# Kernel tuning notes

Measured on AMD Instinct MI355X. Metric: run time of the kernel, lower is better.

## Reference

```python
import jax, jax.numpy as jnp
import numpy as np
import math

K = 10  # args.k, hardcoded in order_topk/fast_topk

def sinusoid_pe(seq_len, d_model, dtype=jnp.float32):
    # PositionalEmbedding: pe[:,0::2]=sin(pos*div), pe[:,1::2]=cos(pos*div)
    pos = jnp.arange(seq_len, dtype=jnp.float32)[:, None]
    div = jnp.exp(jnp.arange(0, d_model, 2, dtype=jnp.float32) * (-math.log(10000.0) / d_model))
    ang = pos * div  # [S, d_model//2]
    pe = jnp.zeros((seq_len, d_model), dtype=jnp.float32)
    pe = pe.at[:, 0::2].set(jnp.sin(ang)).at[:, 1::2].set(jnp.cos(ang))
    return pe.astype(dtype)


def setup_inputs() -> dict:
    key = jax.random.key(0)
    ks = jax.random.split(key, 5)
    B, D, S = 128, 512, 512
    scale1 = 1.0 / math.sqrt(2 * D)
    scale2 = 1.0 / math.sqrt(D)
    return {
        "x": jax.random.normal(ks[0], (B, D, S), dtype=jnp.float32),
        "w1": jax.random.normal(ks[1], (2 * D, D), dtype=jnp.float32) * scale1,
        "b1": jax.random.normal(ks[2], (D,), dtype=jnp.float32) * scale1,
        "w2": jax.random.normal(ks[3], (D, 1), dtype=jnp.float32) * scale2,
        "b2": jax.random.normal(ks[4], (1,), dtype=jnp.float32) * scale2,
    }


def reference(x, w1, b1, w2, b2):
    # x: [B, D, S] -> feature: [B, S, D]  (Sampler: x = x.transpose(-1,-2))
    feat = jnp.swapaxes(x, -1, -2)
    B, S, D = feat.shape
    # shot == 1 branch: per-video mean over tokens, broadcast over seq
    info_g = jnp.broadcast_to(feat.mean(axis=-2, keepdims=True), feat.shape)
    h = jnp.concatenate([feat, info_g], axis=-1)  # [B, S, 2D]
    # evaluator: PositionalEmbedding(1024) -> Linear(1024,512) -> ReLU -> Linear(512,1)
    h = h + sinusoid_pe(S, 2 * D, h.dtype)[None]
    score = jax.nn.relu(jnp.einsum('bsf,fd->bsd', h, w1) + b1)
    score = (jnp.einsum('bsd,do->bso', score, w2) + b2)[..., 0]  # [B, S]
    mn = score.min(axis=1, keepdims=True)
    mx = score.max(axis=1, keepdims=True)
    norm_score = (score - mn) / (mx - mn + 1e-4)
    # fast_topk (eval path): top-k indices, sorted ascending, one-hot selection
    _, idx = jax.lax.top_k(norm_score, K)      # [B, K]
    idx = jnp.sort(idx, axis=-1)
    # torch: one_hot -> [B,K,S], .transpose(-1,-2) -> [B,S,K], then indices.transpose(-1,-2) -> [B,K,S]
    indices = jax.nn.one_hot(idx, S, dtype=feat.dtype)  # [B, K, S]
    selected_feature = jnp.einsum('bks,bsd->bkd', indices, feat)  # bmm gather
    return indices, selected_feature, feat
```

## Files before the change

kernel.cpp:

```cpp
#include <hip/hip_runtime.h>
#include <math.h>

#define B 128
#define D 512
#define S 512
#define TOPK 10

typedef short bf16x8 __attribute__((ext_vector_type(8)));
typedef unsigned short u16x8 __attribute__((ext_vector_type(8)));
typedef float f32x4 __attribute__((ext_vector_type(4)));


__device__ __forceinline__ unsigned splitf(float f) {
    unsigned u = __float_as_uint(f);
    unsigned rb = u + 0x7FFFu + ((u >> 16) & 1u);
    float hf = __uint_as_float(rb & 0xFFFF0000u);
    unsigned u2 = __float_as_uint(f - hf);
    return (rb >> 16) | (u2 & 0xFFFF0000u);
}

__device__ __forceinline__ size_t w1t_base(int d, int k) {
    return (size_t)(((d >> 8) * 32 + (k >> 5)) * 4 + ((k >> 3) & 3)) * 4096 +
           (size_t)(d & 255) * 16 + (k & 7);
}

__global__ __launch_bounds__(512) void fused_stage1(
    const float* __restrict__ x, float* __restrict__ feat, float* __restrict__ g_part,
    ushort* __restrict__ peh, ushort* __restrict__ pel,
    const float* __restrict__ w1, ushort* __restrict__ w1tsw) {
    __shared__ float tile[64 * 129];
    int bid = (int)blockIdx.x;
    int t = threadIdx.x;

    if (bid < 4096) {
        int b = bid >> 5;
        int d0 = ((bid >> 3) & 3) * 128;
        int sblk = bid & 7;
        int s0 = sblk * 64;
        int ty = t >> 4, tx = t & 15;
        const float4* x4 = (const float4*)(x + (size_t)b * D * S);
        float psum[4];
#pragma unroll
        for (int q = 0; q < 4; ++q) {
            int d = ty + 32 * q;
            float4 v = x4[(size_t)(d0 + d) * (S / 4) + (s0 >> 2) + tx];
            tile[d + (4 * tx + 0) * 129] = v.x;
            tile[d + (4 * tx + 1) * 129] = v.y;
            tile[d + (4 * tx + 2) * 129] = v.z;
            tile[d + (4 * tx + 3) * 129] = v.w;
            float sm = (v.x + v.y) + (v.z + v.w);
#pragma unroll
            for (int off = 8; off; off >>= 1) sm += __shfl_down(sm, off, 16);
            psum[q] = sm;
        }
        if (tx == 0) {
            float* gp = g_part + (size_t)sblk * 65536 + b * D + d0;
#pragma unroll
            for (int q = 0; q < 4; ++q) gp[ty + 32 * q] = psum[q] * (1.0f / S);
        }
        __syncthreads();
        int fx = t & 31, sy = t >> 5;
        float* fbase = feat + (size_t)b * S * D + d0 + 4 * fx;
#pragma unroll
        for (int j = 0; j < 4; ++j) {
            int s = sy + 16 * j;
            f32x4 o;
            o[0] = tile[(4 * fx + 0) + s * 129];
            o[1] = tile[(4 * fx + 1) + s * 129];
            o[2] = tile[(4 * fx + 2) + s * 129];
            o[3] = tile[(4 * fx + 3) + s * 129];
            __builtin_nontemporal_store(o, (f32x4*)(fbase + (size_t)(s0 + s) * D));
        }
    } else if (bid < 4608) {
        int s = bid - 4096;
        int i = t;
        float ei = expf((float)(2 * i) * -0.0089944730195f);
        float ang = (float)s * ei;
        float sv = sinf(ang), cv = cosf(ang);
        unsigned ps = splitf(sv), pc = splitf(cv);
        size_t base = (size_t)s * 1024 + 2 * i;
        peh[base] = (ushort)(ps & 0xFFFFu);
        peh[base + 1] = (ushort)(pc & 0xFFFFu);
        pel[base] = (ushort)(ps >> 16);
        pel[base + 1] = (ushort)(pc >> 16);
    } else {
        int id2 = bid - 4608;
        int rp = id2 & 1, tt = id2 >> 1;
        int m = t & 255;
        int c0 = (t >> 8) * 2;
        int d = rp * 256 + m;
        int hs = (m >> 2) & 1;
        ushort* outp = w1tsw + (size_t)(rp * 32 + tt) * 16384 + (size_t)m * 16;
#pragma unroll
        for (int cc = 0; cc < 2; ++cc) {
            int c = c0 + cc;
            u16x8 hi, lo;
#pragma unroll
            for (int j = 0; j < 8; ++j) {
                unsigned p = splitf(w1[(size_t)(tt * 32 + c * 8 + j) * D + d]);
                hi[j] = (ushort)(p & 0xFFFFu);
                lo[j] = (ushort)(p >> 16);
            }
            *(u16x8*)(outp + c * 4096 + hs * 8) = hi;
            *(u16x8*)(outp + c * 4096 + (hs ^ 1) * 8) = lo;
        }
    }
}

#define CP 40
__global__ __launch_bounds__(256) void fused_stage2(
    const float* __restrict__ g_part, const float* __restrict__ w1,
    float* __restrict__ gterm, float* __restrict__ score,
    const ushort* __restrict__ peh, const ushort* __restrict__ pel,
    const ushort* __restrict__ w1tsw, const float* __restrict__ b1,
    float* __restrict__ C1) {
    __shared__ short smemS[4 * 64 * CP];
    int bid = (int)blockIdx.x;
    int t = threadIdx.x;

    if (bid < 256) {
        score[bid * 256 + t] = 0.0f;
        int b = bid >> 1, half = bid & 1;
        float* gs = (float*)smemS;
#pragma unroll
        for (int h = 0; h < 2; ++h) {
            int k = h * 256 + t;
            float acc = 0.f;
#pragma unroll
            for (int sb = 0; sb < 8; ++sb) acc += g_part[(size_t)sb * 65536 + b * D + k];
            gs[k] = acc;
        }
        __syncthreads();
        int d = half * 256 + t;
        float a0 = 0.f, a1 = 0.f, a2 = 0.f, a3 = 0.f;
        for (int k = 0; k < 512; k += 4) {
            a0 += gs[k + 0] * w1[(size_t)(D + k + 0) * D + d];
            a1 += gs[k + 1] * w1[(size_t)(D + k + 1) * D + d];
            a2 += gs[k + 2] * w1[(size_t)(D + k + 2) * D + d];
            a3 += gs[k + 3] * w1[(size_t)(D + k + 3) * D + d];
        }
        gterm[b * D + d] = (a0 + a1) + (a2 + a3);
    } else {
        int cid = bid - 256;
        int d0 = (cid & 7) * 64, s0 = (cid >> 3) * 64;
        short* sAh = smemS;
        short* sAl = smemS + 64 * CP;
        short* sBh = smemS + 2 * 64 * CP;
        short* sBl = smemS + 3 * 64 * CP;
        int w = t >> 6, l = t & 63, lc = l & 15, lg = l >> 4;
        int tm = t >> 2, tk = (t & 3) * 8;
        int bhs = (tm >> 2) & 1;
        f32x4 acc[4] = {};
        for (int k0 = 0; k0 < 1024; k0 += 32) {
            __syncthreads();
            *(bf16x8*)(sAh + tm * CP + tk) =
                *(const bf16x8*)(peh + (size_t)(s0 + tm) * 1024 + k0 + tk);
            *(bf16x8*)(sAl + tm * CP + tk) =
                *(const bf16x8*)(pel + (size_t)(s0 + tm) * 1024 + k0 + tk);
            size_t boff = w1t_base(d0 + tm, k0 + tk);
            *(bf16x8*)(sBh + tm * CP + tk) = *(const bf16x8*)(w1tsw + boff + bhs * 8);
            *(bf16x8*)(sBl + tm * CP + tk) = *(const bf16x8*)(w1tsw + boff + (bhs ^ 1) * 8);
            __syncthreads();
            int m = w * 16 + lc;
            bf16x8 ah = *(const bf16x8*)(sAh + m * CP + lg * 8);
            bf16x8 al = *(const bf16x8*)(sAl + m * CP + lg * 8);
#pragma unroll
            for (int j = 0; j < 4; ++j) {
                int n = j * 16 + lc;
                bf16x8 bh = *(const bf16x8*)(sBh + n * CP + lg * 8);
                bf16x8 bl = *(const bf16x8*)(sBl + n * CP + lg * 8);
                acc[j] = __builtin_amdgcn_mfma_f32_16x16x32_bf16(ah, bh, acc[j], 0, 0, 0);
                acc[j] = __builtin_amdgcn_mfma_f32_16x16x32_bf16(ah, bl, acc[j], 0, 0, 0);
                acc[j] = __builtin_amdgcn_mfma_f32_16x16x32_bf16(al, bh, acc[j], 0, 0, 0);
            }
        }
#pragma unroll
        for (int j = 0; j < 4; ++j)
#pragma unroll
            for (int reg = 0; reg < 4; ++reg) {
                int sg = s0 + w * 16 + lg * 4 + reg;
                int dg = d0 + j * 16 + lc;
                C1[(size_t)sg * D + dg] = acc[j][reg] + b1[dg];
            }
    }
}

__device__ __forceinline__ void gload16(const void* src, void* dst) {
    __builtin_amdgcn_global_load_lds((const __attribute__((address_space(1))) void*)src,
                                     (__attribute__((address_space(3))) void*)dst, 16, 0, 0);
}

__device__ __forceinline__ void split_write(short* sAbuf, int am, int ahalf,
                                            float4 a0, float4 a1, float4 a2, float4 a3) {
    int hs = (am >> 2) & 1;
#pragma unroll
    for (int cc = 0; cc < 2; ++cc) {
        float e0, e1, e2, e3, e4, e5, e6, e7;
        if (cc == 0) {
            e0 = a0.x; e1 = a0.y; e2 = a0.z; e3 = a0.w;
            e4 = a1.x; e5 = a1.y; e6 = a1.z; e7 = a1.w;
        } else {
            e0 = a2.x; e1 = a2.y; e2 = a2.z; e3 = a2.w;
            e4 = a3.x; e5 = a3.y; e6 = a3.z; e7 = a3.w;
        }
        unsigned p0 = splitf(e0), p1 = splitf(e1), p2 = splitf(e2), p3 = splitf(e3);
        unsigned p4 = splitf(e4), p5 = splitf(e5), p6 = splitf(e6), p7 = splitf(e7);
        u16x8 hi, lo;
        hi[0] = (ushort)(p0 & 0xFFFFu); lo[0] = (ushort)(p0 >> 16);
        hi[1] = (ushort)(p1 & 0xFFFFu); lo[1] = (ushort)(p1 >> 16);
        hi[2] = (ushort)(p2 & 0xFFFFu); lo[2] = (ushort)(p2 >> 16);
        hi[3] = (ushort)(p3 & 0xFFFFu); lo[3] = (ushort)(p3 >> 16);
        hi[4] = (ushort)(p4 & 0xFFFFu); lo[4] = (ushort)(p4 >> 16);
        hi[5] = (ushort)(p5 & 0xFFFFu); lo[5] = (ushort)(p5 >> 16);
        hi[6] = (ushort)(p6 & 0xFFFFu); lo[6] = (ushort)(p6 >> 16);
        hi[7] = (ushort)(p7 & 0xFFFFu); lo[7] = (ushort)(p7 >> 16);
        short* dst = sAbuf + (size_t)(2 * ahalf + cc) * 4096 + (size_t)am * 16;
        *(u16x8*)(dst + hs * 8) = hi;
        *(u16x8*)(dst + (hs ^ 1) * 8) = lo;
    }
}

__global__ __launch_bounds__(512, 2) void gemm_mfma(
    const float* __restrict__ feat, const ushort* __restrict__ w1tsw,
    const float* __restrict__ w2, const float* __restrict__ gterm,
    const float* __restrict__ C1, float* __restrict__ score, int row_base) {
    __shared__ short sA[2][4][256][16];
    __shared__ short sB[2][4][256][16];
    int t = threadIdx.x;
    int id = (int)blockIdx.x;
    int lid = (id & 7) * 32 + (id >> 3);
    int rp = lid >> 1, cp = lid & 1;
    int row0 = row_base + (rp << 8);
    int d0 = cp << 8;
    int b = row0 >> 9;

    int am = t & 255, ahalf = t >> 8;
    const float4* asrc = (const float4*)(feat + (size_t)(row0 + am) * D + ahalf * 16);
    const ushort* btile = w1tsw + (size_t)(cp * 32) * 16384;
    int wv = t >> 6, l = t & 63, lc = l & 15, lg = l >> 4;
    int wr = wv >> 1, wc = wv & 1;
    int wbase = (t & ~63);
    int hs = (lc >> 2) & 1;
    int oh = hs * 8, ol = (hs ^ 1) * 8;

    f32x4 acc[4][8] = {};

    {
        float4 a0 = asrc[0], a1 = asrc[1], a2 = asrc[2], a3 = asrc[3];
#pragma unroll
        for (int q = 0; q < 4; ++q)
            gload16(btile + (size_t)(q * 512 + t) * 8,
                    &sB[0][0][0][0] + (size_t)(q * 512 + wbase) * 8);
        split_write(&sA[0][0][0][0], am, ahalf, a0, a1, a2, a3);
    }
    __syncthreads();

    for (int ts = 0; ts < 16; ++ts) {
        int cur = ts & 1, nxt = cur ^ 1;
        float4 a0, a1, a2, a3;
        if (ts < 15) {
            a0 = asrc[(ts + 1) * 8 + 0];
            a1 = asrc[(ts + 1) * 8 + 1];
            a2 = asrc[(ts + 1) * 8 + 2];
            a3 = asrc[(ts + 1) * 8 + 3];
#pragma unroll
            for (int q = 0; q < 4; ++q)
                gload16(btile + (size_t)(ts + 1) * 16384 + (size_t)(q * 512 + t) * 8,
                        &sB[nxt][0][0][0] + (size_t)(q * 512 + wbase) * 8);
        }
        bf16x8 ahf[4], alf[4];
#pragma unroll
        for (int i = 0; i < 4; ++i) {
            const short* ap = &sA[cur][lg][wr * 64 + i * 16 + lc][0];
            ahf[i] = *(const bf16x8*)(ap + oh);
            alf[i] = *(const bf16x8*)(ap + ol);
        }
        __builtin_amdgcn_s_setprio(1);
#pragma unroll
        for (int j = 0; j < 8; ++j) {
            const short* bp = &sB[cur][lg][wc * 128 + j * 16 + lc][0];
            bf16x8 bh = *(const bf16x8*)(bp + oh);
            bf16x8 bl = *(const bf16x8*)(bp + ol);
#pragma unroll
            for (int i = 0; i < 4; ++i) {
                acc[i][j] = __builtin_amdgcn_mfma_f32_16x16x32_bf16(ahf[i], bh, acc[i][j], 0, 0, 0);
                acc[i][j] = __builtin_amdgcn_mfma_f32_16x16x32_bf16(ahf[i], bl, acc[i][j], 0, 0, 0);
                acc[i][j] = __builtin_amdgcn_mfma_f32_16x16x32_bf16(alf[i], bh, acc[i][j], 0, 0, 0);
            }
        }
        __builtin_amdgcn_s_setprio(0);
        if (ts < 15) split_write(&sA[nxt][0][0][0], am, ahalf, a0, a1, a2, a3);
        __syncthreads();
    }

    float w2v[8], gt[8];
#pragma unroll
    for (int j = 0; j < 8; ++j) {
        int d = d0 + wc * 128 + j * 16 + lc;
        w2v[j] = w2[d];
        gt[j] = gterm[b * D + d];
    }
#pragma unroll
    for (int i = 0; i < 4; ++i)
#pragma unroll
        for (int reg = 0; reg < 4; ++reg) {
            int srow = row0 + wr * 64 + i * 16 + lg * 4 + reg;
            int s = srow & 511;
            float part = 0.f;
#pragma unroll
            for (int j = 0; j < 8; ++j) {
                int d = d0 + wc * 128 + j * 16 + lc;
                float z = acc[i][j][reg] + gt[j] + C1[(size_t)s * D + d];
                part += w2v[j] * fmaxf(z, 0.f);
            }
#pragma unroll
            for (int off = 8; off; off >>= 1) part += __shfl_down(part, off, 16);
            if (lc == 0) atomicAdd(&score[srow], part);
        }
}

__global__ void topk_kernel(const float* __restrict__ score, const float* __restrict__ feat,
                            float* __restrict__ out_ind, float* __restrict__ out_sel) {
    __shared__ float work[512];
    __shared__ float wvv[8];
    __shared__ int wii[8];
    __shared__ int topi[TOPK];
    int b = blockIdx.x, t = threadIdx.x;
    work[t] = score[b * S + t];
    __syncthreads();
    for (int it = 0; it < TOPK; ++it) {
        float v = work[t];
        int i = t;
#pragma unroll
        for (int off = 32; off; off >>= 1) {
            float ov = __shfl_down(v, off);
            int oi = __shfl_down(i, off);
            if (ov > v || (ov == v && oi < i)) { v = ov; i = oi; }
        }
        if ((t & 63) == 0) { wvv[t >> 6] = v; wii[t >> 6] = i; }
        __syncthreads();
        if (t == 0) {
            float bv = wvv[0];
            int bi = wii[0];
            for (int w = 1; w < 8; ++w)
                if (wvv[w] > bv || (wvv[w] == bv && wii[w] < bi)) { bv = wvv[w]; bi = wii[w]; }
            topi[it] = bi;
            work[bi] = -INFINITY;
        }
        __syncthreads();
    }
    if (t == 0) {
        for (int a = 1; a < TOPK; ++a) {
            int key = topi[a];
            int c = a - 1;
            while (c >= 0 && topi[c] > key) { topi[c + 1] = topi[c]; --c; }
            topi[c + 1] = key;
        }
    }
    __syncthreads();
    if (t < 128) {
        float4* oi4 = (float4*)(out_ind + (size_t)b * TOPK * S);
        float4* os4 = (float4*)(out_sel + (size_t)b * TOPK * D);
        const float4* fb4 = (const float4*)(feat + (size_t)b * S * D);
#pragma unroll
        for (int k = 0; k < TOPK; ++k) {
            int idx = topi[k];
            float4 ohv;
            ohv.x = (4 * t + 0 == idx) ? 1.0f : 0.0f;
            ohv.y = (4 * t + 1 == idx) ? 1.0f : 0.0f;
            ohv.z = (4 * t + 2 == idx) ? 1.0f : 0.0f;
            ohv.w = (4 * t + 3 == idx) ? 1.0f : 0.0f;
            oi4[k * (S / 4) + t] = ohv;
            os4[k * (D / 4) + t] = fb4[(size_t)idx * (D / 4) + t];
        }
    }
}

extern "C" void kernel_launch(void* const* d_in, const int* in_sizes, int n_in,
                              void* d_out, int out_size, void* d_ws, size_t ws_size,
                              hipStream_t stream) {
    const float* x  = (const float*)d_in[0];
    const float* w1 = (const float*)d_in[1];
    const float* b1 = (const float*)d_in[2];
    const float* w2 = (const float*)d_in[3];

    float* out = (float*)d_out;
    float* out_ind = out;
    float* out_sel = out + (size_t)B * TOPK * S;
    float* feat    = out + 2 * (size_t)B * TOPK * S;

    float* ws      = (float*)d_ws;
    float* score   = ws;
    float* gterm   = ws + 65536;
    float* g_part  = ws + 131072;
    float* C1      = ws + 655360;
    ushort* w1tsw  = (ushort*)(ws + 917504);
    ushort* peh    = (ushort*)(ws + 1441792);
    ushort* pel    = (ushort*)(ws + 1703936);

    fused_stage1<<<4672, 512, 0, stream>>>(x, feat, g_part, peh, pel, w1, w1tsw);
    fused_stage2<<<320, 256, 0, stream>>>(g_part, w1, gterm, score, peh, pel, w1tsw, b1, C1);
    gemm_mfma<<<256, 512, 0, stream>>>(feat, w1tsw, w2, gterm, C1, score, 0);
    gemm_mfma<<<256, 512, 0, stream>>>(feat, w1tsw, w2, gterm, C1, score, 32768);
    topk_kernel<<<B, 512, 0, stream>>>(score, feat, out_ind, out_sel);
}
```

Baseline: 406.3 us.

## Load GEMM A operand directly into registers, drop A shared-memory staging, merge launches

The GEMM kernel no longer stages the feature (A) tile through LDS. Each wave now loads its own 32 rows straight from global memory into registers and splits them into bf16 hi/lo fragments in place. The wave tiling changes from 4x8 to 2x16 MFMA tiles, so every wave covers all 256 columns and reads B from LDS. This removes the LDS writes and reads for A and halves LDS use, and the two half-size launches are merged into one 512-block launch. The cost is uncoalesced, stride-D global loads for A, more LDS B reads per MFMA, and the split conversion repeated per wave. The PE table now uses sincosf in place of separate sin and cos calls.

```diff
diff --git a/kernel.cpp b/kernel.cpp
--- a/kernel.cpp
+++ b/kernel.cpp
@@ -76,7 +76,8 @@
         int i = t;
         float ei = expf((float)(2 * i) * -0.0089944730195f);
         float ang = (float)s * ei;
-        float sv = sinf(ang), cv = cosf(ang);
+        float sv, cv;
+        sincosf(ang, &sv, &cv);
         unsigned ps = splitf(sv), pc = splitf(cv);
         size_t base = (size_t)s * 1024 + 2 * i;
         peh[base] = (ushort)(ps & 0xFFFFu);
@@ -190,126 +191,101 @@
                                      (__attribute__((address_space(3))) void*)dst, 16, 0, 0);
 }
 
-__device__ __forceinline__ void split_write(short* sAbuf, int am, int ahalf,
-                                            float4 a0, float4 a1, float4 a2, float4 a3) {
-    int hs = (am >> 2) & 1;
-#pragma unroll
-    for (int cc = 0; cc < 2; ++cc) {
-        float e0, e1, e2, e3, e4, e5, e6, e7;
-        if (cc == 0) {
-            e0 = a0.x; e1 = a0.y; e2 = a0.z; e3 = a0.w;
-            e4 = a1.x; e5 = a1.y; e6 = a1.z; e7 = a1.w;
-        } else {
-            e0 = a2.x; e1 = a2.y; e2 = a2.z; e3 = a2.w;
-            e4 = a3.x; e5 = a3.y; e6 = a3.z; e7 = a3.w;
-        }
-        unsigned p0 = splitf(e0), p1 = splitf(e1), p2 = splitf(e2), p3 = splitf(e3);
-        unsigned p4 = splitf(e4), p5 = splitf(e5), p6 = splitf(e6), p7 = splitf(e7);
-        u16x8 hi, lo;
-        hi[0] = (ushort)(p0 & 0xFFFFu); lo[0] = (ushort)(p0 >> 16);
-        hi[1] = (ushort)(p1 & 0xFFFFu); lo[1] = (ushort)(p1 >> 16);
-        hi[2] = (ushort)(p2 & 0xFFFFu); lo[2] = (ushort)(p2 >> 16);
-        hi[3] = (ushort)(p3 & 0xFFFFu); lo[3] = (ushort)(p3 >> 16);
-        hi[4] = (ushort)(p4 & 0xFFFFu); lo[4] = (ushort)(p4 >> 16);
-        hi[5] = (ushort)(p5 & 0xFFFFu); lo[5] = (ushort)(p5 >> 16);
-        hi[6] = (ushort)(p6 & 0xFFFFu); lo[6] = (ushort)(p6 >> 16);
-        hi[7] = (ushort)(p7 & 0xFFFFu); lo[7] = (ushort)(p7 >> 16);
-        short* dst = sAbuf + (size_t)(2 * ahalf + cc) * 4096 + (size_t)am * 16;
-        *(u16x8*)(dst + hs * 8) = hi;
-        *(u16x8*)(dst + (hs ^ 1) * 8) = lo;
-    }
-}
-
 __global__ __launch_bounds__(512, 2) void gemm_mfma(
     const float* __restrict__ feat, const ushort* __restrict__ w1tsw,
     const float* __restrict__ w2, const float* __restrict__ gterm,
-    const float* __restrict__ C1, float* __restrict__ score, int row_base) {
-    __shared__ short sA[2][4][256][16];
+    const float* __restrict__ C1, float* __restrict__ score) {
     __shared__ short sB[2][4][256][16];
     int t = threadIdx.x;
     int id = (int)blockIdx.x;
-    int lid = (id & 7) * 32 + (id >> 3);
+    int lid = (id & 7) * 64 + (id >> 3);
     int rp = lid >> 1, cp = lid & 1;
-    int row0 = row_base + (rp << 8);
+    int row0 = rp << 8;
     int d0 = cp << 8;
     int b = row0 >> 9;
 
-    int am = t & 255, ahalf = t >> 8;
-    const float4* asrc = (const float4*)(feat + (size_t)(row0 + am) * D + ahalf * 16);
     const ushort* btile = w1tsw + (size_t)(cp * 32) * 16384;
     int wv = t >> 6, l = t & 63, lc = l & 15, lg = l >> 4;
-    int wr = wv >> 1, wc = wv & 1;
     int wbase = (t & ~63);
     int hs = (lc >> 2) & 1;
     int oh = hs * 8, ol = (hs ^ 1) * 8;
 
-    f32x4 acc[4][8] = {};
-
-    {
-        float4 a0 = asrc[0], a1 = asrc[1], a2 = asrc[2], a3 = asrc[3];
-#pragma unroll
-        for (int q = 0; q < 4; ++q)
-            gload16(btile + (size_t)(q * 512 + t) * 8,
-                    &sB[0][0][0][0] + (size_t)(q * 512 + wbase) * 8);
-        split_write(&sA[0][0][0][0], am, ahalf, a0, a1, a2, a3);
-    }
+    const float* aptr = feat + (size_t)(row0 + wv * 32 + lc) * D + lg * 8;
+
+    f32x4 acc[2][16] = {};
+    f32x4 av[2][2];
+
+    av[0][0] = *(const f32x4*)(aptr);
+    av[0][1] = *(const f32x4*)(aptr + 4);
+    av[1][0] = *(const f32x4*)(aptr + 16 * D);
+    av[1][1] = *(const f32x4*)(aptr + 16 * D + 4);
+#pragma unroll
+    for (int q = 0; q < 4; ++q)
+        gload16(btile + (size_t)(q * 512 + t) * 8,
+                &sB[0][0][0][0] + (size_t)(q * 512 + wbase) * 8);
     __syncthreads();
 
     for (int ts = 0; ts < 16; ++ts) {
         int cur = ts & 1, nxt = cur ^ 1;
-        float4 a0, a1, a2, a3;
+        f32x4 avn[2][2];
         if (ts < 15) {
-            a0 = asrc[(ts + 1) * 8 + 0];
-            a1 = asrc[(ts + 1) * 8 + 1];
-            a2 = asrc[(ts + 1) * 8 + 2];
-            a3 = asrc[(ts + 1) * 8 + 3];
+            const float* ap = aptr + (ts + 1) * 32;
+            avn[0][0] = *(const f32x4*)(ap);
+            avn[0][1] = *(const f32x4*)(ap + 4);
+            avn[1][0] = *(const f32x4*)(ap + 16 * D);
+            avn[1][1] = *(const f32x4*)(ap + 16 * D + 4);
 #pragma unroll
             for (int q = 0; q < 4; ++q)
                 gload16(btile + (size_t)(ts + 1) * 16384 + (size_t)(q * 512 + t) * 8,
                         &sB[nxt][0][0][0] + (size_t)(q * 512 + wbase) * 8);
         }
-        bf16x8 ahf[4], alf[4];
-#pragma unroll
-        for (int i = 0; i < 4; ++i) {
-            const short* ap = &sA[cur][lg][wr * 64 + i * 16 + lc][0];
-            ahf[i] = *(const bf16x8*)(ap + oh);
-            alf[i] = *(const bf16x8*)(ap + ol);
-        }
+        bf16x8 ahf[2], alf[2];
+#pragma unroll
+        for (int i = 0; i < 2; ++i)
+#pragma unroll
+            for (int e = 0; e < 8; ++e) {
+                unsigned p = splitf(av[i][e >> 2][e & 3]);
+                ahf[i][e] = (short)(p & 0xFFFFu);
+                alf[i][e] = (short)(p >> 16);
+            }
         __builtin_amdgcn_s_setprio(1);
 #pragma unroll
-        for (int j = 0; j < 8; ++j) {
-            const short* bp = &sB[cur][lg][wc * 128 + j * 16 + lc][0];
+        for (int j = 0; j < 16; ++j) {
+            const short* bp = &sB[cur][lg][j * 16 + lc][0];
             bf16x8 bh = *(const bf16x8*)(bp + oh);
             bf16x8 bl = *(const bf16x8*)(bp + ol);
 #pragma unroll
-            for (int i = 0; i < 4; ++i) {
+            for (int i = 0; i < 2; ++i) {
                 acc[i][j] = __builtin_amdgcn_mfma_f32_16x16x32_bf16(ahf[i], bh, acc[i][j], 0, 0, 0);
                 acc[i][j] = __builtin_amdgcn_mfma_f32_16x16x32_bf16(ahf[i], bl, acc[i][j], 0, 0, 0);
                 acc[i][j] = __builtin_amdgcn_mfma_f32_16x16x32_bf16(alf[i], bh, acc[i][j], 0, 0, 0);
             }
         }
         __builtin_amdgcn_s_setprio(0);
-        if (ts < 15) split_write(&sA[nxt][0][0][0], am, ahalf, a0, a1, a2, a3);
-        __syncthreads();
-    }
-
-    float w2v[8], gt[8];
-#pragma unroll
-    for (int j = 0; j < 8; ++j) {
-        int d = d0 + wc * 128 + j * 16 + lc;
+        if (ts < 15) {
+            av[0][0] = avn[0][0]; av[0][1] = avn[0][1];
+            av[1][0] = avn[1][0]; av[1][1] = avn[1][1];
+        }
+        __syncthreads();
+    }
+
+    float w2v[16], gt[16];
+#pragma unroll
+    for (int j = 0; j < 16; ++j) {
+        int d = d0 + j * 16 + lc;
         w2v[j] = w2[d];
         gt[j] = gterm[b * D + d];
     }
 #pragma unroll
-    for (int i = 0; i < 4; ++i)
+    for (int i = 0; i < 2; ++i)
 #pragma unroll
         for (int reg = 0; reg < 4; ++reg) {
-            int srow = row0 + wr * 64 + i * 16 + lg * 4 + reg;
+            int srow = row0 + wv * 32 + i * 16 + lg * 4 + reg;
             int s = srow & 511;
             float part = 0.f;
 #pragma unroll
-            for (int j = 0; j < 8; ++j) {
-                int d = d0 + wc * 128 + j * 16 + lc;
+            for (int j = 0; j < 16; ++j) {
+                int d = d0 + j * 16 + lc;
                 float z = acc[i][j][reg] + gt[j] + C1[(size_t)s * D + d];
                 part += w2v[j] * fmaxf(z, 0.f);
             }
@@ -400,7 +376,6 @@
 
     fused_stage1<<<4672, 512, 0, stream>>>(x, feat, g_part, peh, pel, w1, w1tsw);
     fused_stage2<<<320, 256, 0, stream>>>(g_part, w1, gterm, score, peh, pel, w1tsw, b1, C1);
-    gemm_mfma<<<256, 512, 0, stream>>>(feat, w1tsw, w2, gterm, C1, score, 0);
-    gemm_mfma<<<256, 512, 0, stream>>>(feat, w1tsw, w2, gterm, C1, score, 32768);
+    gemm_mfma<<<512, 512, 0, stream>>>(feat, w1tsw, w2, gterm, C1, score);
     topk_kernel<<<B, 512, 0, stream>>>(score, feat, out_ind, out_sel);
 }
```

Result: faster. 387.6 us (-4.6%).
